# Kernel tuning notes

Measured on AMD Instinct MI355X. Metric: run time of the kernel, lower is better.

Reference implementation:

```python
import jax, jax.numpy as jnp
import numpy as np

N, E, F = 50000, 800000, 64


def _lin_init(key, fan_in, fan_out):
    k1, k2 = jax.random.split(key)
    bound = 1.0 / np.sqrt(fan_in)
    W = jax.random.uniform(k1, (fan_in, fan_out), minval=-bound, maxval=bound, dtype=jnp.float32)
    b = jax.random.uniform(k2, (fan_out,), minval=-bound, maxval=bound, dtype=jnp.float32)
    return W, b


def setup_inputs() -> dict:
    key = jax.random.key(0)
    ks = jax.random.split(key, 16)
    inp = {
        'node_attr': jax.random.normal(ks[0], (N, 3), dtype=jnp.float32),
        'edge_attr': jax.random.normal(ks[1], (E, 3), dtype=jnp.float32),
        'edge_index': jax.random.randint(ks[2], (2, E), 0, N, dtype=jnp.int32),
    }
    # conv1: in = 2*3 + 3 = 9
    inp['c1_W1'], inp['c1_b1'] = _lin_init(ks[3], 9, F)
    inp['c1_W2'], inp['c1_b2'] = _lin_init(ks[4], F, F)
    # conv2: in = 2*F + (F + 3)
    inp['c2_W1'], inp['c2_b1'] = _lin_init(ks[5], 2 * F + F + 3, F)
    inp['c2_W2'], inp['c2_b2'] = _lin_init(ks[6], F, F)
    # conv3/conv4: in = 2*(2F) + 2F = 6F
    inp['c3_W1'], inp['c3_b1'] = _lin_init(ks[7], 6 * F, F)
    inp['c3_W2'], inp['c3_b2'] = _lin_init(ks[8], F, F)
    inp['c4_W1'], inp['c4_b1'] = _lin_init(ks[9], 6 * F, F)
    inp['c4_W2'], inp['c4_b2'] = _lin_init(ks[10], F, F)
    # head mlp: F -> 64 -> 3
    inp['m_W1'], inp['m_b1'] = _lin_init(ks[11], F, 64)
    inp['m_W2'], inp['m_b2'] = _lin_init(ks[12], 64, 3)
    return inp


def _edge_conv(x, row, col, e_attr, W1, b1, W2, b2):
    # gather -> concat -> 2-layer MLP on edges
    h = jnp.concatenate([x[row], x[col], e_attr], axis=1)  # [E, 2*Dn + De]
    edge_out = jax.nn.relu(h @ W1 + b1) @ W2 + b2          # [E, F]
    # scatter-mean back to source nodes
    s = jax.ops.segment_sum(edge_out, row, num_segments=x.shape[0])
    cnt = jax.ops.segment_sum(jnp.ones((row.shape[0],), edge_out.dtype), row, num_segments=x.shape[0])
    node_out = s / jnp.maximum(cnt, 1.0)[:, None]
    return node_out, edge_out


def reference(node_attr, edge_attr, edge_index,
              c1_W1, c1_b1, c1_W2, c1_b2,
              c2_W1, c2_b1, c2_W2, c2_b2,
              c3_W1, c3_b1, c3_W2, c3_b2,
              c4_W1, c4_b1, c4_W2, c4_b2,
              m_W1, m_b1, m_W2, m_b2):
    row, col = edge_index[0], edge_index[1]
    relu = jax.nn.relu

    x1, e1 = _edge_conv(node_attr, row, col, edge_attr, c1_W1, c1_b1, c1_W2, c1_b2)
    x1, e1 = relu(x1), relu(e1)

    x2, e2 = _edge_conv(x1, row, col, jnp.concatenate([e1, edge_attr], axis=1),
                        c2_W1, c2_b1, c2_W2, c2_b2)
    x2, e2 = relu(x2), relu(e2)

    x_ll, x_l = x1, x2
    e_ll, e_l = e1, e2
    for (W1, b1, W2, b2) in ((c3_W1, c3_b1, c3_W2, c3_b2), (c4_W1, c4_b1, c4_W2, c4_b2)):
        x_cur, e_cur = _edge_conv(jnp.concatenate([x_l, x_ll], axis=1), row, col,
                                  jnp.concatenate([e_l, e_ll], axis=1), W1, b1, W2, b2)
        x_cur, e_cur = relu(x_cur), relu(e_cur)
        x_ll, x_l = x_l, x_cur
        e_ll, e_l = e_l, e_cur

    x = relu(x_l @ m_W1 + m_b1) @ m_W2 + m_b2  # [N, 3]
    return (x, e_l)
```

## Files before the change

kernel.cpp:

```cpp
#include <hip/hip_runtime.h>
#include <cstdint>
#include <cstddef>


#define NN 50000
#define NE 800000
#define GRID_EC 512

typedef _Float16 f16;
typedef _Float16 f16x8 __attribute__((ext_vector_type(8)));
typedef _Float16 f16x4 __attribute__((ext_vector_type(4)));
typedef float    f32x4 __attribute__((ext_vector_type(4)));

__global__ void count_kernel(const int* __restrict__ eidx, int* __restrict__ cnt) {
  int i = blockIdx.x * 256 + threadIdx.x;
  if (i < NE) atomicAdd(&cnt[eidx[i]], 1);
}

__global__ void scan_a(const int* __restrict__ cnt, int* __restrict__ bsum) {
  __shared__ int sh[256];
  int i = blockIdx.x * 256 + threadIdx.x;
  sh[threadIdx.x] = (i < NN) ? cnt[i] : 0;
  __syncthreads();
  for (int off = 128; off > 0; off >>= 1) {
    if (threadIdx.x < off) sh[threadIdx.x] += sh[threadIdx.x + off];
    __syncthreads();
  }
  if (threadIdx.x == 0) bsum[blockIdx.x] = sh[0];
}

__global__ void scan_b(const int* __restrict__ bsum, int* __restrict__ boff, int nb) {
  __shared__ int sh[256];
  int t = threadIdx.x;
  int v = (t < nb) ? bsum[t] : 0;
  sh[t] = v; __syncthreads();
  for (int off = 1; off < 256; off <<= 1) {
    int x = (t >= off) ? sh[t - off] : 0;
    __syncthreads();
    sh[t] += x;
    __syncthreads();
  }
  if (t < nb) boff[t] = sh[t] - v;
}

__global__ void scan_c(const int* __restrict__ cnt, const int* __restrict__ boff,
                       int* __restrict__ start, int* __restrict__ cursor) {
  __shared__ int sh[256];
  int t = threadIdx.x;
  int i = blockIdx.x * 256 + t;
  int v = (i < NN) ? cnt[i] : 0;
  sh[t] = v; __syncthreads();
  for (int off = 1; off < 256; off <<= 1) {
    int x = (t >= off) ? sh[t - off] : 0;
    __syncthreads();
    sh[t] += x;
    __syncthreads();
  }
  if (i < NN) {
    int ex = boff[blockIdx.x] + sh[t] - v;
    start[i] = ex; cursor[i] = ex;
  }
  if (i == 0) start[NN] = NE;
}

__global__ void scatter_kernel(const int* __restrict__ eidx, const float* __restrict__ ea,
                               int* __restrict__ cursor,
                               int* __restrict__ srow, int* __restrict__ scol,
                               int* __restrict__ perm, f16* __restrict__ ea4) {
  int e = blockIdx.x * 256 + threadIdx.x;
  if (e >= NE) return;
  int r = eidx[e];
  int j = atomicAdd(&cursor[r], 1);
  srow[j] = r;
  scol[j] = eidx[NE + e];
  perm[j] = e;
  f16x4 v;
  v[0] = (f16)ea[3 * (size_t)e];
  v[1] = (f16)ea[3 * (size_t)e + 1];
  v[2] = (f16)ea[3 * (size_t)e + 2];
  v[3] = (f16)0.0f;
  *(f16x4*)&ea4[4 * (size_t)j] = v;
}

__global__ void prep_kernel(const float* __restrict__ W1, int kreal1, int ksteps1,
                            const float* __restrict__ W2,
                            f16* __restrict__ w1f, f16* __restrict__ w2f) {
  int u = blockIdx.x * 256 + threadIdx.x;
  int total1 = ksteps1 * 256;
  const float* W; f16* dst; int kreal, slot;
  if (u < total1)            { W = W1; dst = w1f; kreal = kreal1; slot = u; }
  else if (u < total1 + 512) { W = W2; dst = w2f; kreal = 64;     slot = u - total1; }
  else return;
  int l = slot & 63, t = (slot >> 6) & 3, ks = slot >> 8;
  int n  = t * 16 + (l & 15);
  int kb = ks * 32 + ((l >> 4) * 8);
  f16x8 v;
#pragma unroll
  for (int j = 0; j < 8; ++j) {
    int k = kb + j;
    v[j] = (f16)((k < kreal) ? W[k * 64 + n] : 0.0f);
  }
  *(f16x8*)&dst[slot * 8] = v;
}

template<int F32OUT>
__global__ void node_sum_kernel(const f16* __restrict__ eout, const int* __restrict__ start,
                                void* __restrict__ xout) {
  int v = blockIdx.x * 4 + (threadIdx.x >> 6);
  int lane = threadIdx.x & 63;
  int g = lane >> 4, c4 = (lane & 15) * 4;
  int s0 = start[v], s1 = start[v + 1];
  f32x4 acc = (f32x4){0.f, 0.f, 0.f, 0.f};
  for (int i = s0 + g; i < s1; i += 4) {
    f16x4 h = *(const f16x4*)&eout[(size_t)i * 64 + c4];
#pragma unroll
    for (int q = 0; q < 4; ++q) acc[q] += (float)h[q];
  }
#pragma unroll
  for (int q = 0; q < 4; ++q) {
    acc[q] += __shfl_xor(acc[q], 16, 64);
    acc[q] += __shfl_xor(acc[q], 32, 64);
  }
  int cv = s1 - s0;
  float inv = 1.0f / (float)(cv > 0 ? cv : 1);
  if (g == 0) {
    if (F32OUT) {
      f32x4 o;
#pragma unroll
      for (int q = 0; q < 4; ++q) o[q] = fmaxf(acc[q] * inv, 0.0f);
      *(f32x4*)&((float*)xout)[(size_t)v * 64 + c4] = o;
    } else {
      f16x4 o;
#pragma unroll
      for (int q = 0; q < 4; ++q) o[q] = (f16)fmaxf(acc[q] * inv, 0.0f);
      *(f16x4*)&((f16*)xout)[(size_t)v * 64 + c4] = o;
    }
  }
}

template<int CONV>
__global__ __launch_bounds__(256, 2) void edge_conv_kernel(
    const int* __restrict__ srow, const int* __restrict__ scol,
    const int* __restrict__ perm,
    const float* __restrict__ na,
    const f16* __restrict__ xA, const f16* __restrict__ xB,
    const f16* __restrict__ eA, const f16* __restrict__ eB,
    const f16* __restrict__ ea4,
    const f16* __restrict__ w1f, const f16* __restrict__ w2f,
    const float* __restrict__ b1, const float* __restrict__ b2,
    f16* __restrict__ eout, float* __restrict__ out_e)
{
  constexpr int KSTEPS = (CONV == 1) ? 1 : (CONV == 2 ? 7 : 12);

  __shared__ f16 w1s[KSTEPS * 2048];
  __shared__ __align__(16) f16 hbuf[4][16][72];

  const int tid  = threadIdx.x;
  const int lane = tid & 63;
  const int wv   = tid >> 6;
  const int quad = lane >> 4;
  const int l15  = lane & 15;

  for (int u = tid; u < KSTEPS * 256; u += 256)
    *(f16x8*)&w1s[u * 8] = *(const f16x8*)&w1f[u * 8];

  float bb1[4], bb2[4];
#pragma unroll
  for (int t = 0; t < 4; ++t) { bb1[t] = b1[t * 16 + l15]; bb2[t] = b2[t * 16 + l15]; }

  f16x8 w2r[2][4];
#pragma unroll
  for (int kk = 0; kk < 2; ++kk)
#pragma unroll
    for (int t = 0; t < 4; ++t)
      w2r[kk][t] = *(const f16x8*)&w2f[((kk * 4 + t) * 64 + lane) * 8];

  __syncthreads();

  constexpr int NTILE = NE / 32;
  const int gw = blockIdx.x * 4 + wv;

  for (int jt = gw; jt < NTILE; jt += GRID_EC * 4) {
    const int jb = jt * 32;
    const int j0 = jb + l15, j1 = j0 + 16;

    f32x4 acc[2][4];
#pragma unroll
    for (int s = 0; s < 2; ++s)
#pragma unroll
      for (int t = 0; t < 4; ++t) acc[s][t] = (f32x4){0.f, 0.f, 0.f, 0.f};

    if constexpr (CONV == 1) {
      const int r0 = srow[j0], r1 = srow[j1];
      const int c0 = scol[j0], c1 = scol[j1];
      f16x8 a0, a1;
#pragma unroll
      for (int j = 0; j < 8; ++j) { a0[j] = (f16)0.0f; a1[j] = (f16)0.0f; }
      f16x4 q0 = *(const f16x4*)&ea4[4 * (size_t)j0];
      f16x4 q1 = *(const f16x4*)&ea4[4 * (size_t)j1];
      if (quad == 0) {
        a0[0] = (f16)na[r0*3];  a0[1] = (f16)na[r0*3+1];  a0[2] = (f16)na[r0*3+2];
        a0[3] = (f16)na[c0*3];  a0[4] = (f16)na[c0*3+1];  a0[5] = (f16)na[c0*3+2];
        a0[6] = q0[0];          a0[7] = q0[1];
        a1[0] = (f16)na[r1*3];  a1[1] = (f16)na[r1*3+1];  a1[2] = (f16)na[r1*3+2];
        a1[3] = (f16)na[c1*3];  a1[4] = (f16)na[c1*3+1];  a1[5] = (f16)na[c1*3+2];
        a1[6] = q1[0];          a1[7] = q1[1];
      } else if (quad == 1) {
        a0[0] = q0[2];
        a1[0] = q1[2];
      }
#pragma unroll
      for (int t = 0; t < 4; ++t) {
        f16x8 b = *(const f16x8*)&w1s[(t * 64 + lane) * 8];
        acc[0][t] = __builtin_amdgcn_mfma_f32_16x16x32_f16(a0, b, acc[0][t], 0, 0, 0);
        acc[1][t] = __builtin_amdgcn_mfma_f32_16x16x32_f16(a1, b, acc[1][t], 0, 0, 0);
      }
    } else {
      constexpr int NREG = (CONV == 2) ? 3 : 6;
      constexpr int ERCH = (CONV == 2) ? 2 : 4;
      const int r0 = srow[j0], r1 = srow[j1];
      const int c0 = scol[j0], c1 = scol[j1];
      const f16* p0[NREG]; const f16* p1[NREG];
      if constexpr (CONV == 2) {
        p0[0] = xA + (size_t)r0 * 64;  p1[0] = xA + (size_t)r1 * 64;
        p0[1] = xA + (size_t)c0 * 64;  p1[1] = xA + (size_t)c1 * 64;
        p0[2] = eA + (size_t)j0 * 64;  p1[2] = eA + (size_t)j1 * 64;
      } else {
        p0[0] = xA + (size_t)r0 * 64;  p1[0] = xA + (size_t)r1 * 64;
        p0[1] = xB + (size_t)r0 * 64;  p1[1] = xB + (size_t)r1 * 64;
        p0[2] = xA + (size_t)c0 * 64;  p1[2] = xA + (size_t)c1 * 64;
        p0[3] = xB + (size_t)c0 * 64;  p1[3] = xB + (size_t)c1 * 64;
        p0[4] = eA + (size_t)j0 * 64;  p1[4] = eA + (size_t)j1 * 64;
        p0[5] = eB + (size_t)j0 * 64;  p1[5] = eB + (size_t)j1 * 64;
      }
#pragma unroll
      for (int ks = 0; ks < NREG * 2; ++ks) {
        const int c = ks >> 1, kk = ks & 1;
        f16x8 a0 = *(const f16x8*)(p0[c] + kk * 32 + quad * 8);
        f16x8 a1 = *(const f16x8*)(p1[c] + kk * 32 + quad * 8);
        if (c >= ERCH) {
#pragma unroll
          for (int j = 0; j < 8; ++j) {
            a0[j] = (a0[j] > (f16)0.0f) ? a0[j] : (f16)0.0f;
            a1[j] = (a1[j] > (f16)0.0f) ? a1[j] : (f16)0.0f;
          }
        }
#pragma unroll
        for (int t = 0; t < 4; ++t) {
          f16x8 b = *(const f16x8*)&w1s[((ks * 4 + t) * 64 + lane) * 8];
          acc[0][t] = __builtin_amdgcn_mfma_f32_16x16x32_f16(a0, b, acc[0][t], 0, 0, 0);
          acc[1][t] = __builtin_amdgcn_mfma_f32_16x16x32_f16(a1, b, acc[1][t], 0, 0, 0);
        }
      }
      if constexpr (CONV == 2) {
        f16x8 a0, a1;
#pragma unroll
        for (int j = 0; j < 8; ++j) { a0[j] = (f16)0.0f; a1[j] = (f16)0.0f; }
        f16x4 q0 = *(const f16x4*)&ea4[4 * (size_t)j0];
        f16x4 q1 = *(const f16x4*)&ea4[4 * (size_t)j1];
        if (quad == 0) {
          a0[0] = q0[0]; a0[1] = q0[1]; a0[2] = q0[2];
          a1[0] = q1[0]; a1[1] = q1[1]; a1[2] = q1[2];
        }
#pragma unroll
        for (int t = 0; t < 4; ++t) {
          f16x8 b = *(const f16x8*)&w1s[((6 * 4 + t) * 64 + lane) * 8];
          acc[0][t] = __builtin_amdgcn_mfma_f32_16x16x32_f16(a0, b, acc[0][t], 0, 0, 0);
          acc[1][t] = __builtin_amdgcn_mfma_f32_16x16x32_f16(a1, b, acc[1][t], 0, 0, 0);
        }
      }
    }

#pragma unroll
    for (int s = 0; s < 2; ++s) {
#pragma unroll
      for (int t = 0; t < 4; ++t)
#pragma unroll
        for (int r = 0; r < 4; ++r)
          hbuf[wv][quad * 4 + r][t * 16 + l15] = (f16)fmaxf(acc[s][t][r] + bb1[t], 0.0f);

      f32x4 a2[4];
#pragma unroll
      for (int t = 0; t < 4; ++t) a2[t] = (f32x4){0.f, 0.f, 0.f, 0.f};
#pragma unroll
      for (int kk = 0; kk < 2; ++kk) {
        f16x8 ah = *(const f16x8*)&hbuf[wv][l15][kk * 32 + quad * 8];
#pragma unroll
        for (int t = 0; t < 4; ++t)
          a2[t] = __builtin_amdgcn_mfma_f32_16x16x32_f16(ah, w2r[kk][t], a2[t], 0, 0, 0);
      }

#pragma unroll
      for (int t = 0; t < 4; ++t)
#pragma unroll
        for (int r = 0; r < 4; ++r)
          hbuf[wv][quad * 4 + r][t * 16 + l15] = (f16)(a2[t][r] + bb2[t]);

      const int j = jb + s * 16 + l15;
      f16x8 lo = *(const f16x8*)&hbuf[wv][l15][quad * 8];
      f16x8 hi = *(const f16x8*)&hbuf[wv][l15][32 + quad * 8];
      *(f16x8*)&eout[(size_t)j * 64 + quad * 8] = lo;
      *(f16x8*)&eout[(size_t)j * 64 + 32 + quad * 8] = hi;

      if constexpr (CONV == 4) {
#pragma unroll
        for (int r = 0; r < 4; ++r) {
          const int p = perm[jb + s * 16 + quad * 4 + r];
#pragma unroll
          for (int t = 0; t < 4; ++t)
            out_e[(size_t)p * 64 + t * 16 + l15] = fmaxf(a2[t][r] + bb2[t], 0.0f);
        }
      }
    }
  }
}

__global__ void head_kernel(const float* __restrict__ x4,
                            const float* __restrict__ W1, const float* __restrict__ b1,
                            const float* __restrict__ W2, const float* __restrict__ b2,
                            float* __restrict__ out) {
  __shared__ float xs[4][64];
  __shared__ float hs[4][64];
  int tid = threadIdx.x;
  int i = tid >> 6, f = tid & 63;
  int nb = blockIdx.x * 4;
  xs[i][f] = x4[(size_t)(nb + i) * 64 + f];
  __syncthreads();
  float h = b1[f];
#pragma unroll
  for (int k = 0; k < 64; ++k) h += xs[i][k] * W1[k * 64 + f];
  hs[i][f] = fmaxf(h, 0.0f);
  __syncthreads();
  if (tid < 12) {
    int ii = tid / 3, j = tid % 3;
    float o = b2[j];
#pragma unroll
    for (int k = 0; k < 64; ++k) o += hs[ii][k] * W2[k * 3 + j];
    out[(size_t)(nb + ii) * 3 + j] = o;
  }
}

extern "C" void kernel_launch(void* const* d_in, const int* in_sizes, int n_in,
                              void* d_out, int out_size, void* d_ws, size_t ws_size,
                              hipStream_t stream) {
  const float* na   = (const float*)d_in[0];
  const float* ea   = (const float*)d_in[1];
  const int*   eidx = (const int*)d_in[2];
  const float* c1W1 = (const float*)d_in[3];
  const float* c1b1 = (const float*)d_in[4];
  const float* c1W2 = (const float*)d_in[5];
  const float* c1b2 = (const float*)d_in[6];
  const float* c2W1 = (const float*)d_in[7];
  const float* c2b1 = (const float*)d_in[8];
  const float* c2W2 = (const float*)d_in[9];
  const float* c2b2 = (const float*)d_in[10];
  const float* c3W1 = (const float*)d_in[11];
  const float* c3b1 = (const float*)d_in[12];
  const float* c3W2 = (const float*)d_in[13];
  const float* c3b2 = (const float*)d_in[14];
  const float* c4W1 = (const float*)d_in[15];
  const float* c4b1 = (const float*)d_in[16];
  const float* c4W2 = (const float*)d_in[17];
  const float* c4b2 = (const float*)d_in[18];
  const float* mW1  = (const float*)d_in[19];
  const float* mb1  = (const float*)d_in[20];
  const float* mW2  = (const float*)d_in[21];
  const float* mb2  = (const float*)d_in[22];

  char* ws = (char*)d_ws;
  size_t off = 0;
  auto alloc = [&](size_t b) -> void* {
    void* p = ws + off;
    off += (b + 255) & ~(size_t)255;
    return p;
  };
  int*   cnt    = (int*)alloc((size_t)NN * 4);
  int*   bsum   = (int*)alloc(256 * 4);
  int*   boff   = (int*)alloc(256 * 4);
  int*   start  = (int*)alloc((size_t)(NN + 1) * 4);
  int*   cursor = (int*)alloc((size_t)NN * 4);
  int*   srow   = (int*)alloc((size_t)NE * 4);
  int*   scol   = (int*)alloc((size_t)NE * 4);
  int*   perm   = (int*)alloc((size_t)NE * 4);
  f16*   ea4    = (f16*)alloc((size_t)NE * 4 * 2);
  f16*   x1     = (f16*)alloc((size_t)NN * 64 * 2);
  f16*   x2     = (f16*)alloc((size_t)NN * 64 * 2);
  f16*   x3     = (f16*)alloc((size_t)NN * 64 * 2);
  float* x4     = (float*)alloc((size_t)NN * 64 * 4);
  f16*   se1    = (f16*)alloc((size_t)NE * 64 * 2);
  f16*   se2    = (f16*)alloc((size_t)NE * 64 * 2);
  f16*   se3    = (f16*)alloc((size_t)NE * 64 * 2);
  f16*   w1f1 = (f16*)alloc((size_t) 1 * 2048 * 2);
  f16*   w1f2 = (f16*)alloc((size_t) 7 * 2048 * 2);
  f16*   w1f3 = (f16*)alloc((size_t)12 * 2048 * 2);
  f16*   w1f4 = (f16*)alloc((size_t)12 * 2048 * 2);
  f16*   w2f1 = (f16*)alloc((size_t)4096 * 2);
  f16*   w2f2 = (f16*)alloc((size_t)4096 * 2);
  f16*   w2f3 = (f16*)alloc((size_t)4096 * 2);
  f16*   w2f4 = (f16*)alloc((size_t)4096 * 2);

  float* out_x = (float*)d_out;
  float* out_e = out_x + (size_t)NN * 3;

  constexpr int NBS = (NN + 255) / 256;

  hipMemsetAsync(cnt, 0, (size_t)NN * 4, stream);
  count_kernel<<<NE / 256, 256, 0, stream>>>(eidx, cnt);
  scan_a<<<NBS, 256, 0, stream>>>(cnt, bsum);
  scan_b<<<1, 256, 0, stream>>>(bsum, boff, NBS);
  scan_c<<<NBS, 256, 0, stream>>>(cnt, boff, start, cursor);
  scatter_kernel<<<NE / 256, 256, 0, stream>>>(eidx, ea, cursor, srow, scol, perm, ea4);

  prep_kernel<<< 3, 256, 0, stream>>>(c1W1,   9,  1, c1W2, w1f1, w2f1);
  prep_kernel<<< 9, 256, 0, stream>>>(c2W1, 195,  7, c2W2, w1f2, w2f2);
  prep_kernel<<<14, 256, 0, stream>>>(c3W1, 384, 12, c3W2, w1f3, w2f3);
  prep_kernel<<<14, 256, 0, stream>>>(c4W1, 384, 12, c4W2, w1f4, w2f4);

  edge_conv_kernel<1><<<GRID_EC, 256, 0, stream>>>(srow, scol, nullptr, na,
      nullptr, nullptr, nullptr, nullptr, ea4, w1f1, w2f1, c1b1, c1b2, se1, nullptr);
  node_sum_kernel<0><<<NN / 4, 256, 0, stream>>>(se1, start, x1);

  edge_conv_kernel<2><<<GRID_EC, 256, 0, stream>>>(srow, scol, nullptr, nullptr,
      x1, nullptr, se1, nullptr, ea4, w1f2, w2f2, c2b1, c2b2, se2, nullptr);
  node_sum_kernel<0><<<NN / 4, 256, 0, stream>>>(se2, start, x2);

  edge_conv_kernel<3><<<GRID_EC, 256, 0, stream>>>(srow, scol, nullptr, nullptr,
      x2, x1, se2, se1, nullptr, w1f3, w2f3, c3b1, c3b2, se3, nullptr);
  node_sum_kernel<0><<<NN / 4, 256, 0, stream>>>(se3, start, x3);

  edge_conv_kernel<4><<<GRID_EC, 256, 0, stream>>>(srow, scol, perm, nullptr,
      x3, x2, se3, se2, nullptr, w1f4, w2f4, c4b1, c4b2, se1, out_e);
  node_sum_kernel<1><<<NN / 4, 256, 0, stream>>>(se1, start, x4);

  head_kernel<<<NN / 4, 256, 0, stream>>>(x4, mW1, mb1, mW2, mb2, out_x);
}
```

Before: 980.6 us.

## Cap LDS weight staging and halve hbuf to raise edge-conv occupancy

Stages at most 8 K-steps of W1 in LDS and reads the remaining K-steps (conv3/conv4) straight from global/L2 memory. The per-wave transpose buffer shrinks to 32 columns, with the relu/bias hidden and output tiles round-tripped in two halves. Launch bounds go to 4 blocks per CU and the grid doubles, aiming for more waves in flight to hide gather latency. The cost is extra global weight loads in the inner MFMA loop, a tighter register budget that may spill, and more LDS round trips.

```diff
diff --git a/kernel.cpp b/kernel.cpp
--- a/kernel.cpp
+++ b/kernel.cpp
@@ -5,7 +5,7 @@
 
 #define NN 50000
 #define NE 800000
-#define GRID_EC 512
+#define GRID_EC 1024
 
 typedef _Float16 f16;
 typedef _Float16 f16x8 __attribute__((ext_vector_type(8)));
@@ -139,7 +139,7 @@
 }
 
 template<int CONV>
-__global__ __launch_bounds__(256, 2) void edge_conv_kernel(
+__global__ __launch_bounds__(256, 4) void edge_conv_kernel(
     const int* __restrict__ srow, const int* __restrict__ scol,
     const int* __restrict__ perm,
     const float* __restrict__ na,
@@ -151,9 +151,10 @@
     f16* __restrict__ eout, float* __restrict__ out_e)
 {
   constexpr int KSTEPS = (CONV == 1) ? 1 : (CONV == 2 ? 7 : 12);
-
-  __shared__ f16 w1s[KSTEPS * 2048];
-  __shared__ __align__(16) f16 hbuf[4][16][72];
+  constexpr int LDS_KS = (KSTEPS > 8) ? 8 : KSTEPS;
+
+  __shared__ f16 w1s[LDS_KS * 2048];
+  __shared__ __align__(16) f16 hbuf[4][16][40];
 
   const int tid  = threadIdx.x;
   const int lane = tid & 63;
@@ -161,7 +162,7 @@
   const int quad = lane >> 4;
   const int l15  = lane & 15;
 
-  for (int u = tid; u < KSTEPS * 256; u += 256)
+  for (int u = tid; u < LDS_KS * 256; u += 256)
     *(f16x8*)&w1s[u * 8] = *(const f16x8*)&w1f[u * 8];
 
   float bb1[4], bb2[4];
@@ -176,6 +177,11 @@
       w2r[kk][t] = *(const f16x8*)&w2f[((kk * 4 + t) * 64 + lane) * 8];
 
   __syncthreads();
+
+  auto bfrag = [&](int ks, int t) -> f16x8 {
+    if (ks < LDS_KS) return *(const f16x8*)&w1s[((ks * 4 + t) * 64 + lane) * 8];
+    return *(const f16x8*)&w1f[((ks * 4 + t) * 64 + lane) * 8];
+  };
 
   constexpr int NTILE = NE / 32;
   const int gw = blockIdx.x * 4 + wv;
@@ -211,7 +217,7 @@
       }
 #pragma unroll
       for (int t = 0; t < 4; ++t) {
-        f16x8 b = *(const f16x8*)&w1s[(t * 64 + lane) * 8];
+        f16x8 b = bfrag(0, t);
         acc[0][t] = __builtin_amdgcn_mfma_f32_16x16x32_f16(a0, b, acc[0][t], 0, 0, 0);
         acc[1][t] = __builtin_amdgcn_mfma_f32_16x16x32_f16(a1, b, acc[1][t], 0, 0, 0);
       }
@@ -247,7 +253,7 @@
         }
 #pragma unroll
         for (int t = 0; t < 4; ++t) {
-          f16x8 b = *(const f16x8*)&w1s[((ks * 4 + t) * 64 + lane) * 8];
+          f16x8 b = bfrag(ks, t);
           acc[0][t] = __builtin_amdgcn_mfma_f32_16x16x32_f16(a0, b, acc[0][t], 0, 0, 0);
           acc[1][t] = __builtin_amdgcn_mfma_f32_16x16x32_f16(a1, b, acc[1][t], 0, 0, 0);
         }
@@ -264,7 +270,7 @@
         }
 #pragma unroll
         for (int t = 0; t < 4; ++t) {
-          f16x8 b = *(const f16x8*)&w1s[((6 * 4 + t) * 64 + lane) * 8];
+          f16x8 b = bfrag(6, t);
           acc[0][t] = __builtin_amdgcn_mfma_f32_16x16x32_f16(a0, b, acc[0][t], 0, 0, 0);
           acc[1][t] = __builtin_amdgcn_mfma_f32_16x16x32_f16(a1, b, acc[1][t], 0, 0, 0);
         }
@@ -273,34 +279,39 @@
 
 #pragma unroll
     for (int s = 0; s < 2; ++s) {
-#pragma unroll
-      for (int t = 0; t < 4; ++t)
-#pragma unroll
-        for (int r = 0; r < 4; ++r)
-          hbuf[wv][quad * 4 + r][t * 16 + l15] = (f16)fmaxf(acc[s][t][r] + bb1[t], 0.0f);
-
       f32x4 a2[4];
 #pragma unroll
       for (int t = 0; t < 4; ++t) a2[t] = (f32x4){0.f, 0.f, 0.f, 0.f};
 #pragma unroll
       for (int kk = 0; kk < 2; ++kk) {
-        f16x8 ah = *(const f16x8*)&hbuf[wv][l15][kk * 32 + quad * 8];
+#pragma unroll
+        for (int th = 0; th < 2; ++th) {
+          const int t = kk * 2 + th;
+#pragma unroll
+          for (int r = 0; r < 4; ++r)
+            hbuf[wv][quad * 4 + r][th * 16 + l15] = (f16)fmaxf(acc[s][t][r] + bb1[t], 0.0f);
+        }
+        f16x8 ah = *(const f16x8*)&hbuf[wv][l15][quad * 8];
 #pragma unroll
         for (int t = 0; t < 4; ++t)
           a2[t] = __builtin_amdgcn_mfma_f32_16x16x32_f16(ah, w2r[kk][t], a2[t], 0, 0, 0);
       }
 
-#pragma unroll
-      for (int t = 0; t < 4; ++t)
-#pragma unroll
-        for (int r = 0; r < 4; ++r)
-          hbuf[wv][quad * 4 + r][t * 16 + l15] = (f16)(a2[t][r] + bb2[t]);
-
       const int j = jb + s * 16 + l15;
-      f16x8 lo = *(const f16x8*)&hbuf[wv][l15][quad * 8];
-      f16x8 hi = *(const f16x8*)&hbuf[wv][l15][32 + quad * 8];
-      *(f16x8*)&eout[(size_t)j * 64 + quad * 8] = lo;
-      *(f16x8*)&eout[(size_t)j * 64 + 32 + quad * 8] = hi;
+      f16x8 oh[2];
+#pragma unroll
+      for (int h = 0; h < 2; ++h) {
+#pragma unroll
+        for (int th = 0; th < 2; ++th) {
+          const int t = h * 2 + th;
+#pragma unroll
+          for (int r = 0; r < 4; ++r)
+            hbuf[wv][quad * 4 + r][th * 16 + l15] = (f16)(a2[t][r] + bb2[t]);
+        }
+        oh[h] = *(const f16x8*)&hbuf[wv][l15][quad * 8];
+      }
+      *(f16x8*)&eout[(size_t)j * 64 + quad * 8] = oh[0];
+      *(f16x8*)&eout[(size_t)j * 64 + 32 + quad * 8] = oh[1];
 
       if constexpr (CONV == 4) {
 #pragma unroll
```

Result: slower. 1.366 ms (+39.3%).
